# Kernel tuning notes

Measured on AMD Instinct MI355X. Metric: run time of the kernel, lower is better.

Reference implementation:

```python
import jax, jax.numpy as jnp
import numpy as np
import math

B, N, T, F_IN, F_OUT = 8, 512, 12, 32, 64


def setup_inputs() -> dict:
    key = jax.random.key(0)
    k1, k2, k3, k4, k5 = jax.random.split(key, 5)
    x = jax.random.normal(k1, (B, N, T, F_IN), dtype=jnp.float32)
    phaseAct_matrix = jax.random.uniform(k2, (B, T, N, N), dtype=jnp.float32)
    adj = jax.random.uniform(k3, (N, N), dtype=jnp.float32)  # sym-normalized adjacency stand-in
    mask = (jax.random.uniform(k4, (N,)) < 0.5).astype(jnp.float32)  # 1 = observed node, 0 = unknown
    theta = jax.random.normal(k5, (F_IN, F_OUT), dtype=jnp.float32) * 0.05
    return {"x": x, "phaseAct_matrix": phaseAct_matrix, "adj": adj, "mask": mask, "theta": theta}


def _spatial_attention(x):
    # x: (B, N, T, F) -> scores (B, T, N, N)
    f = x.shape[-1]
    xt = x.transpose(0, 2, 1, 3)  # (B, T, N, F)
    score = jnp.einsum('btnf,btmf->btnm', xt, xt) / math.sqrt(f)
    return jax.nn.softmax(score, axis=-1)


def reference(x, phaseAct_matrix, adj, mask, theta):
    f = x.shape[-1]
    t_steps = x.shape[2]
    inv_sqrt_f = 1.0 / math.sqrt(f)
    m = mask[None, :, None, None]  # broadcast over (B, N, T-1, F)

    def body(i, x_cur):
        sa = _spatial_attention(x_cur) * inv_sqrt_f          # (B, T, N, N)
        sat_act = (phaseAct_matrix * sa).transpose(0, 1, 3, 2)  # (B, T, N, N) transposed
        xt = x_cur.transpose(0, 2, 1, 3)                     # (B, T, N, F)
        # predict step t from step t-1: (B, T-1, N, F)
        x_pred = jnp.einsum('btnm,btmf->btnf', sat_act[:, 1:], xt[:, :t_steps - 1])
        x_pred = x_pred.transpose(0, 2, 1, 3)                # (B, N, T-1, F)
        # revise_unknown: keep observed nodes, impute unknown nodes at steps 1..T-1
        x_rev = x_cur[:, :, 1:, :] * m + x_pred * (1.0 - m)
        return jnp.concatenate([x_cur[:, :, 0:1, :], x_rev], axis=2)

    x = jax.lax.fori_loop(1, t_steps, body, x)

    sa = _spatial_attention(x) * inv_sqrt_f                  # (B, T, N, N)
    satAct_adj = phaseAct_matrix * adj[None, None] * sa      # (B, T, N, N)
    xt = x.transpose(0, 2, 1, 3)                             # (B, T, N, F)
    agg = jnp.einsum('btmn,btmf->btnf', satAct_adj, xt)      # transpose(adj) @ x
    out = jax.nn.relu(jnp.einsum('btnf,fo->btno', agg, theta))  # (B, T, N, F_out)
    return out.transpose(0, 2, 1, 3)                         # (B, N, T, F_out)
```

## Files before the change

kernel.cpp:

```cpp
#include <hip/hip_runtime.h>


#define B_ 8
#define N_ 512
#define T_ 12
#define F_ 32
#define O_ 64

typedef unsigned int uint_t;
typedef unsigned short ushort_t;
typedef _Float16 f16_t;
typedef _Float16 f16x4 __attribute__((ext_vector_type(4)));
typedef _Float16 f16x8 __attribute__((ext_vector_type(8)));
typedef float f32x4 __attribute__((ext_vector_type(4)));

__device__ __forceinline__ int xidx(int b, int n, int t, int f) {
    return ((b * N_ + n) * T_ + t) * F_ + f;
}
__device__ __forceinline__ f16x8 load_frag8(const float* p) {
    float4 a = *reinterpret_cast<const float4*>(p);
    float4 b = *reinterpret_cast<const float4*>(p + 4);
    f16x8 r;
    r[0] = (f16_t)a.x; r[1] = (f16_t)a.y; r[2] = (f16_t)a.z; r[3] = (f16_t)a.w;
    r[4] = (f16_t)b.x; r[5] = (f16_t)b.y; r[6] = (f16_t)b.z; r[7] = (f16_t)b.w;
    return r;
}
union U2H4 { uint2 u; f16x4 h; };

__global__ __launch_bounds__(256)
void permute_kernel(const float* __restrict__ src, ushort_t* __restrict__ dst)
{
    __shared__ float Lp[32][516];
    const int tid = threadIdx.x;
    const int cp  = blockIdx.x;
    const int s   = blockIdx.y;
    src += (size_t)s * N_ * N_ + (size_t)cp * 32 * N_;
    uint4* dstu = (uint4*)dst + (size_t)s * 32768 + (size_t)cp * 2048;

    #pragma unroll
    for (int k = 0; k < 64; ++k) {
        int idx = tid + 256 * k;
        Lp[idx >> 9][idx & 511] = src[idx];
    }
    __syncthreads();
    #pragma unroll
    for (int k = 0; k < 8; ++k) {
        int u    = tid + 256 * k;
        int nt   = u >> 6;
        int l    = u & 63;
        int quad = l >> 4;
        int cl   = l & 15;
        int n    = nt * 16 + cl;
        int r0   = quad * 4;
        union { f16_t h[2]; uint_t i; } p0, p1, p2, p3;
        p0.h[0] = (f16_t)Lp[r0][n];      p0.h[1] = (f16_t)Lp[r0 + 1][n];
        p1.h[0] = (f16_t)Lp[r0 + 2][n];  p1.h[1] = (f16_t)Lp[r0 + 3][n];
        p2.h[0] = (f16_t)Lp[16 + r0][n];     p2.h[1] = (f16_t)Lp[16 + r0 + 1][n];
        p3.h[0] = (f16_t)Lp[16 + r0 + 2][n]; p3.h[1] = (f16_t)Lp[16 + r0 + 3][n];
        dstu[u] = make_uint4(p0.i, p1.i, p2.i, p3.i);
    }
}

template <int FINAL>
__global__ __launch_bounds__(256, 4)
void stats_kernel(const float* __restrict__ x0,
                  const float* __restrict__ xcur,
                  float2* __restrict__ MS)
{
    const int tid  = threadIdx.x;
    const int w    = tid >> 6;
    const int l    = tid & 63;
    const int quad = l >> 4;
    const int col  = l & 15;
    const int t    = FINAL ? blockIdx.y : blockIdx.y + 1;
    const int b    = blockIdx.z;
    const int mb   = (blockIdx.x * 4 + w) * 16;
    const float inv_f = 0.17677669529663687f;
    const float* xs = (FINAL && t == 0) ? x0 : xcur;

    f16x8 bm = load_frag8(&xs[xidx(b, mb + col, t, quad * 8)]);

    float M[4] = {-1e30f, -1e30f, -1e30f, -1e30f};
    float S[4] = {0.f, 0.f, 0.f, 0.f};
    #pragma unroll 2
    for (int base = 0; base < 8; ++base) {
        #pragma unroll
        for (int ss = 0; ss < 4; ++ss) {
            const int nt2 = base * 4 + ss;
            f16x8 an = load_frag8(&xs[xidx(b, nt2 * 16 + col, t, quad * 8)]);
            f32x4 s4 = __builtin_amdgcn_mfma_f32_16x16x32_f16(
                           an, bm, (f32x4){0.f, 0.f, 0.f, 0.f}, 0, 0, 0);
            float m4 = fmaxf(fmaxf(s4[0], s4[1]), fmaxf(s4[2], s4[3])) * inv_f;
            float Mn = fmaxf(M[ss], m4);
            S[ss] = S[ss] * __expf(M[ss] - Mn)
                  + (__expf(s4[0] * inv_f - Mn) + __expf(s4[1] * inv_f - Mn))
                  + (__expf(s4[2] * inv_f - Mn) + __expf(s4[3] * inv_f - Mn));
            M[ss] = Mn;
        }
    }
    float M01 = fmaxf(M[0], M[1]);
    float S01 = S[0] * __expf(M[0] - M01) + S[1] * __expf(M[1] - M01);
    float M23 = fmaxf(M[2], M[3]);
    float S23 = S[2] * __expf(M[2] - M23) + S[3] * __expf(M[3] - M23);
    float Mm  = fmaxf(M01, M23);
    float Sm  = S01 * __expf(M01 - Mm) + S23 * __expf(M23 - Mm);
    #pragma unroll
    for (int d = 16; d < 64; d <<= 1) {
        float Mo = __shfl_xor(Mm, d, 64), So = __shfl_xor(Sm, d, 64);
        float Mn = fmaxf(Mm, Mo);
        Sm = Sm * __expf(Mm - Mn) + So * __expf(Mo - Mn);
        Mm = Mn;
    }
    if (l < 16)
        MS[(size_t)(b * T_ + t) * N_ + mb + l] = make_float2(Mm, inv_f / Sm);
}

template <int FINAL>
__global__ __launch_bounds__(256, 3)
void pred_kernel(const float* __restrict__ x0,
                 const float* __restrict__ xcur,
                 float* __restrict__ dst,
                 const ushort_t* __restrict__ phase_h,
                 const ushort_t* __restrict__ adj_h,
                 const float* __restrict__ mask,
                 const float2* __restrict__ MS)
{
    const int tid  = threadIdx.x;
    const int w    = tid >> 6;
    const int l    = tid & 63;
    const int quad = l >> 4;
    const int col  = l & 15;
    const int t    = FINAL ? blockIdx.y : blockIdx.y + 1;
    const int b    = blockIdx.z;
    const int nt   = blockIdx.x * 4 + w;
    const float inv_f = 0.17677669529663687f;

    const float* xs     = (FINAL && t == 0) ? x0 : xcur;
    const float* xp_src = FINAL ? xs : ((t == 1) ? x0 : xcur);
    const int    tp     = FINAL ? t : t - 1;

    f16x8 bf = load_frag8(&xs[xidx(b, nt * 16 + col, t, quad * 8)]);
    const uint4* phu4 = (const uint4*)phase_h + (size_t)(b * T_ + t) * 32768
                        + nt * 64 + l;
    const uint4* adu4 = (const uint4*)adj_h + nt * 64 + l;
    const float2* msp = MS + (size_t)(b * T_ + t) * N_ + quad * 4;

    f32x4 acc0 = (f32x4){0.f, 0.f, 0.f, 0.f};
    f32x4 acc1 = (f32x4){0.f, 0.f, 0.f, 0.f};

    #pragma unroll 2
    for (int cp = 0; cp < 16; ++cp) {
        const int mb0 = cp * 32;
        const int mb1 = mb0 + 16;
        uint4 phq = phu4[cp * 2048];
        uint4 ajq;
        if (FINAL) ajq = adu4[cp * 2048];
        f16x8 af0 = load_frag8(&xs[xidx(b, mb0 + col, t, quad * 8)]);
        f16x8 af1 = load_frag8(&xs[xidx(b, mb1 + col, t, quad * 8)]);
        float4 msA0 = *(const float4*)(msp + mb0);
        float4 msB0 = *(const float4*)(msp + mb0 + 2);
        float4 msA1 = *(const float4*)(msp + mb1);
        float4 msB1 = *(const float4*)(msp + mb1 + 2);
        f16x4 bp00, bp01, bp10, bp11;
        #pragma unroll
        for (int jj = 0; jj < 4; ++jj) {
            bp00[jj] = (f16_t)xp_src[xidx(b, mb0 + quad * 4 + jj, tp, col)];
            bp01[jj] = (f16_t)xp_src[xidx(b, mb0 + quad * 4 + jj, tp, 16 + col)];
            bp10[jj] = (f16_t)xp_src[xidx(b, mb1 + quad * 4 + jj, tp, col)];
            bp11[jj] = (f16_t)xp_src[xidx(b, mb1 + quad * 4 + jj, tp, 16 + col)];
        }

        f32x4 s40 = __builtin_amdgcn_mfma_f32_16x16x32_f16(
                        af0, bf, (f32x4){0.f, 0.f, 0.f, 0.f}, 0, 0, 0);
        f32x4 s41 = __builtin_amdgcn_mfma_f32_16x16x32_f16(
                        af1, bf, (f32x4){0.f, 0.f, 0.f, 0.f}, 0, 0, 0);

        U2H4 p0; p0.u = make_uint2(phq.x, phq.y);
        U2H4 p1; p1.u = make_uint2(phq.z, phq.w);
        U2H4 a0, a1;
        if (FINAL) { a0.u = make_uint2(ajq.x, ajq.y); a1.u = make_uint2(ajq.z, ajq.w); }

        const float Mv0[4] = {msA0.x, msA0.z, msB0.x, msB0.z};
        const float Sv0[4] = {msA0.y, msA0.w, msB0.y, msB0.w};
        const float Mv1[4] = {msA1.x, msA1.z, msB1.x, msB1.z};
        const float Sv1[4] = {msA1.y, msA1.w, msB1.y, msB1.w};

        f16x4 wf0, wf1;
        #pragma unroll
        for (int v = 0; v < 4; ++v) {
            float e0 = __expf(s40[v] * inv_f - Mv0[v]) * Sv0[v] * (float)p0.h[v];
            float e1 = __expf(s41[v] * inv_f - Mv1[v]) * Sv1[v] * (float)p1.h[v];
            if (FINAL) { e0 *= (float)a0.h[v]; e1 *= (float)a1.h[v]; }
            wf0[v] = (f16_t)e0;
            wf1[v] = (f16_t)e1;
        }
        acc0 = __builtin_amdgcn_mfma_f32_16x16x16f16(wf0, bp00, acc0, 0, 0, 0);
        acc1 = __builtin_amdgcn_mfma_f32_16x16x16f16(wf0, bp01, acc1, 0, 0, 0);
        acc0 = __builtin_amdgcn_mfma_f32_16x16x16f16(wf1, bp10, acc0, 0, 0, 0);
        acc1 = __builtin_amdgcn_mfma_f32_16x16x16f16(wf1, bp11, acc1, 0, 0, 0);
    }

    #pragma unroll
    for (int v = 0; v < 4; ++v) {
        const int n = nt * 16 + quad * 4 + v;
        if (FINAL) {
            float* d0 = &dst[((size_t)(b * T_ + t) * N_ + n) * F_ + col];
            d0[0]  = acc0[v];
            d0[16] = acc1[v];
        } else {
            const int i0 = xidx(b, n, t, col);
            const float mk = mask[n];
            dst[i0]      = (mk != 0.f) ? xcur[i0]      : acc0[v];
            dst[i0 + 16] = (mk != 0.f) ? xcur[i0 + 16] : acc1[v];
        }
    }
}

__global__ __launch_bounds__(256)
void proj_kernel(const float* __restrict__ agg, const float* __restrict__ theta,
                 float* __restrict__ out)
{
    __shared__ float th[F_ * O_];
    int tid = threadIdx.x;
    #pragma unroll
    for (int p = 0; p < 8; ++p) th[tid + 256 * p] = theta[tid + 256 * p];
    __syncthreads();
    int g  = blockIdx.x * 256 + tid;
    int o  = g & 63;
    int r  = g >> 6;
    int tt = r % T_;
    int r2 = r / T_;
    int n  = r2 & 511;
    int b  = r2 >> 9;
    const float* a = &agg[((b * T_ + tt) * N_ + n) * F_];
    float s = 0.f;
    #pragma unroll
    for (int f = 0; f < F_; ++f) s += a[f] * th[f * O_ + o];
    out[g] = fmaxf(s, 0.f);
}

extern "C" void kernel_launch(void* const* d_in, const int* in_sizes, int n_in,
                              void* d_out, int out_size, void* d_ws, size_t ws_size,
                              hipStream_t stream)
{
    const float* x     = (const float*)d_in[0];
    const float* phase = (const float*)d_in[1];
    const float* adj   = (const float*)d_in[2];
    const float* mask  = (const float*)d_in[3];
    const float* theta = (const float*)d_in[4];
    float* out = (float*)d_out;

    const size_t XE = (size_t)B_ * N_ * T_ * F_;
    float*    xA      = (float*)d_ws;
    float*    xB      = xA + XE;
    float*    agg     = xB + XE;
    ushort_t* phase_h = (ushort_t*)(agg + XE);
    ushort_t* adj_h   = phase_h + (size_t)96 * N_ * N_;
    float2*   MS      = (float2*)(adj_h + (size_t)N_ * N_);

    permute_kernel<<<dim3(16, 96), 256, 0, stream>>>(phase, phase_h);
    permute_kernel<<<dim3(16, 1), 256, 0, stream>>>(adj, adj_h);

    const float* cur = x;
    float* bufs[2] = { xA, xB };
    for (int i = 0; i < T_ - 1; ++i) {
        float* nxt = bufs[i & 1];
        stats_kernel<0><<<dim3(8, T_ - 1, B_), 256, 0, stream>>>(x, cur, MS);
        pred_kernel<0><<<dim3(8, T_ - 1, B_), 256, 0, stream>>>(
            x, cur, nxt, phase_h, adj_h, mask, MS);
        cur = nxt;
    }
    stats_kernel<1><<<dim3(8, T_, B_), 256, 0, stream>>>(x, cur, MS);
    pred_kernel<1><<<dim3(8, T_, B_), 256, 0, stream>>>(
        x, cur, agg, phase_h, adj_h, mask, MS);
    proj_kernel<<<(B_ * N_ * T_ * O_) / 256, 256, 0, stream>>>(agg, theta, out);
}
```

Baseline: 1.007 ms.

## Fuse softmax stats and prediction kernels with shared-memory row statistics

Merges the softmax statistics kernel into the prediction kernel. Each 512-thread block computes max/sum for all rows of its (b,t) slice into shared memory, then runs the aggregation. This removes a launch per iteration and the global round trip for the stats buffer. In exchange, each block recomputes stats redundantly (4 blocks per slice) and the grid gets smaller and serialized per block.

New measurement: 2.068 ms. +105.3%, slower.

```diff
diff --git a/kernel.cpp b/kernel.cpp
--- a/kernel.cpp
+++ b/kernel.cpp
@@ -62,11 +62,16 @@
 }
 
 template <int FINAL>
-__global__ __launch_bounds__(256, 4)
-void stats_kernel(const float* __restrict__ x0,
+__global__ __launch_bounds__(512, 4)
+void fused_kernel(const float* __restrict__ x0,
                   const float* __restrict__ xcur,
-                  float2* __restrict__ MS)
-{
+                  float* __restrict__ dst,
+                  const ushort_t* __restrict__ phase_h,
+                  const ushort_t* __restrict__ adj_h,
+                  const float* __restrict__ mask)
+{
+    __shared__ float2 MSl[N_];
+
     const int tid  = threadIdx.x;
     const int w    = tid >> 6;
     const int l    = tid & 63;
@@ -74,76 +79,58 @@
     const int col  = l & 15;
     const int t    = FINAL ? blockIdx.y : blockIdx.y + 1;
     const int b    = blockIdx.z;
-    const int mb   = (blockIdx.x * 4 + w) * 16;
-    const float inv_f = 0.17677669529663687f;
-    const float* xs = (FINAL && t == 0) ? x0 : xcur;
-
-    f16x8 bm = load_frag8(&xs[xidx(b, mb + col, t, quad * 8)]);
-
-    float M[4] = {-1e30f, -1e30f, -1e30f, -1e30f};
-    float S[4] = {0.f, 0.f, 0.f, 0.f};
-    #pragma unroll 2
-    for (int base = 0; base < 8; ++base) {
-        #pragma unroll
-        for (int ss = 0; ss < 4; ++ss) {
-            const int nt2 = base * 4 + ss;
-            f16x8 an = load_frag8(&xs[xidx(b, nt2 * 16 + col, t, quad * 8)]);
-            f32x4 s4 = __builtin_amdgcn_mfma_f32_16x16x32_f16(
-                           an, bm, (f32x4){0.f, 0.f, 0.f, 0.f}, 0, 0, 0);
-            float m4 = fmaxf(fmaxf(s4[0], s4[1]), fmaxf(s4[2], s4[3])) * inv_f;
-            float Mn = fmaxf(M[ss], m4);
-            S[ss] = S[ss] * __expf(M[ss] - Mn)
-                  + (__expf(s4[0] * inv_f - Mn) + __expf(s4[1] * inv_f - Mn))
-                  + (__expf(s4[2] * inv_f - Mn) + __expf(s4[3] * inv_f - Mn));
-            M[ss] = Mn;
-        }
-    }
-    float M01 = fmaxf(M[0], M[1]);
-    float S01 = S[0] * __expf(M[0] - M01) + S[1] * __expf(M[1] - M01);
-    float M23 = fmaxf(M[2], M[3]);
-    float S23 = S[2] * __expf(M[2] - M23) + S[3] * __expf(M[3] - M23);
-    float Mm  = fmaxf(M01, M23);
-    float Sm  = S01 * __expf(M01 - Mm) + S23 * __expf(M23 - Mm);
-    #pragma unroll
-    for (int d = 16; d < 64; d <<= 1) {
-        float Mo = __shfl_xor(Mm, d, 64), So = __shfl_xor(Sm, d, 64);
-        float Mn = fmaxf(Mm, Mo);
-        Sm = Sm * __expf(Mm - Mn) + So * __expf(Mo - Mn);
-        Mm = Mn;
-    }
-    if (l < 16)
-        MS[(size_t)(b * T_ + t) * N_ + mb + l] = make_float2(Mm, inv_f / Sm);
-}
-
-template <int FINAL>
-__global__ __launch_bounds__(256, 3)
-void pred_kernel(const float* __restrict__ x0,
-                 const float* __restrict__ xcur,
-                 float* __restrict__ dst,
-                 const ushort_t* __restrict__ phase_h,
-                 const ushort_t* __restrict__ adj_h,
-                 const float* __restrict__ mask,
-                 const float2* __restrict__ MS)
-{
-    const int tid  = threadIdx.x;
-    const int w    = tid >> 6;
-    const int l    = tid & 63;
-    const int quad = l >> 4;
-    const int col  = l & 15;
-    const int t    = FINAL ? blockIdx.y : blockIdx.y + 1;
-    const int b    = blockIdx.z;
-    const int nt   = blockIdx.x * 4 + w;
     const float inv_f = 0.17677669529663687f;
 
     const float* xs     = (FINAL && t == 0) ? x0 : xcur;
     const float* xp_src = FINAL ? xs : ((t == 1) ? x0 : xcur);
     const int    tp     = FINAL ? t : t - 1;
 
+    for (int mi = 0; mi < 4; ++mi) {
+        const int mb = (w * 4 + mi) * 16;
+        f16x8 bm = load_frag8(&xs[xidx(b, mb + col, t, quad * 8)]);
+
+        float M[4] = {-1e30f, -1e30f, -1e30f, -1e30f};
+        float S[4] = {0.f, 0.f, 0.f, 0.f};
+        #pragma unroll 2
+        for (int base = 0; base < 8; ++base) {
+            #pragma unroll
+            for (int ss = 0; ss < 4; ++ss) {
+                const int nt2 = base * 4 + ss;
+                f16x8 an = load_frag8(&xs[xidx(b, nt2 * 16 + col, t, quad * 8)]);
+                f32x4 s4 = __builtin_amdgcn_mfma_f32_16x16x32_f16(
+                               an, bm, (f32x4){0.f, 0.f, 0.f, 0.f}, 0, 0, 0);
+                float m4 = fmaxf(fmaxf(s4[0], s4[1]), fmaxf(s4[2], s4[3])) * inv_f;
+                float Mn = fmaxf(M[ss], m4);
+                S[ss] = S[ss] * __expf(M[ss] - Mn)
+                      + (__expf(s4[0] * inv_f - Mn) + __expf(s4[1] * inv_f - Mn))
+                      + (__expf(s4[2] * inv_f - Mn) + __expf(s4[3] * inv_f - Mn));
+                M[ss] = Mn;
+            }
+        }
+        float M01 = fmaxf(M[0], M[1]);
+        float S01 = S[0] * __expf(M[0] - M01) + S[1] * __expf(M[1] - M01);
+        float M23 = fmaxf(M[2], M[3]);
+        float S23 = S[2] * __expf(M[2] - M23) + S[3] * __expf(M[3] - M23);
+        float Mm  = fmaxf(M01, M23);
+        float Sm  = S01 * __expf(M01 - Mm) + S23 * __expf(M23 - Mm);
+        #pragma unroll
+        for (int d = 16; d < 64; d <<= 1) {
+            float Mo = __shfl_xor(Mm, d, 64), So = __shfl_xor(Sm, d, 64);
+            float Mn = fmaxf(Mm, Mo);
+            Sm = Sm * __expf(Mm - Mn) + So * __expf(Mo - Mn);
+            Mm = Mn;
+        }
+        if (l < 16)
+            MSl[mb + l] = make_float2(Mm, inv_f / Sm);
+    }
+    __syncthreads();
+
+    const int nt = blockIdx.x * 8 + w;
     f16x8 bf = load_frag8(&xs[xidx(b, nt * 16 + col, t, quad * 8)]);
     const uint4* phu4 = (const uint4*)phase_h + (size_t)(b * T_ + t) * 32768
                         + nt * 64 + l;
     const uint4* adu4 = (const uint4*)adj_h + nt * 64 + l;
-    const float2* msp = MS + (size_t)(b * T_ + t) * N_ + quad * 4;
+    const float* msp = (const float*)MSl + quad * 8;
 
     f32x4 acc0 = (f32x4){0.f, 0.f, 0.f, 0.f};
     f32x4 acc1 = (f32x4){0.f, 0.f, 0.f, 0.f};
@@ -157,10 +144,10 @@
         if (FINAL) ajq = adu4[cp * 2048];
         f16x8 af0 = load_frag8(&xs[xidx(b, mb0 + col, t, quad * 8)]);
         f16x8 af1 = load_frag8(&xs[xidx(b, mb1 + col, t, quad * 8)]);
-        float4 msA0 = *(const float4*)(msp + mb0);
-        float4 msB0 = *(const float4*)(msp + mb0 + 2);
-        float4 msA1 = *(const float4*)(msp + mb1);
-        float4 msB1 = *(const float4*)(msp + mb1 + 2);
+        float4 msA0 = *(const float4*)(msp + mb0 * 2);
+        float4 msB0 = *(const float4*)(msp + mb0 * 2 + 4);
+        float4 msA1 = *(const float4*)(msp + mb1 * 2);
+        float4 msB1 = *(const float4*)(msp + mb1 * 2 + 4);
         f16x4 bp00, bp01, bp10, bp11;
         #pragma unroll
         for (int jj = 0; jj < 4; ++jj) {
@@ -256,7 +243,6 @@
     float*    agg     = xB + XE;
     ushort_t* phase_h = (ushort_t*)(agg + XE);
     ushort_t* adj_h   = phase_h + (size_t)96 * N_ * N_;
-    float2*   MS      = (float2*)(adj_h + (size_t)N_ * N_);
 
     permute_kernel<<<dim3(16, 96), 256, 0, stream>>>(phase, phase_h);
     permute_kernel<<<dim3(16, 1), 256, 0, stream>>>(adj, adj_h);
@@ -265,13 +251,11 @@
     float* bufs[2] = { xA, xB };
     for (int i = 0; i < T_ - 1; ++i) {
         float* nxt = bufs[i & 1];
-        stats_kernel<0><<<dim3(8, T_ - 1, B_), 256, 0, stream>>>(x, cur, MS);
-        pred_kernel<0><<<dim3(8, T_ - 1, B_), 256, 0, stream>>>(
-            x, cur, nxt, phase_h, adj_h, mask, MS);
+        fused_kernel<0><<<dim3(4, T_ - 1, B_), 512, 0, stream>>>(
+            x, cur, nxt, phase_h, adj_h, mask);
         cur = nxt;
     }
-    stats_kernel<1><<<dim3(8, T_, B_), 256, 0, stream>>>(x, cur, MS);
-    pred_kernel<1><<<dim3(8, T_, B_), 256, 0, stream>>>(
-        x, cur, agg, phase_h, adj_h, mask, MS);
+    fused_kernel<1><<<dim3(4, T_, B_), 512, 0, stream>>>(
+        x, cur, agg, phase_h, adj_h, mask);
     proj_kernel<<<(B_ * N_ * T_ * O_) / 256, 256, 0, stream>>>(agg, theta, out);
 }
```

## Software-pipeline global loads in stats and aggregation kernels with register prefetch

Applied to the files above, without the earlier changes.

The stats kernel now keeps a four-deep ring of x fragments in registers and issues the load for tile nt+4 before the MFMA for tile nt. The aggregation kernel is fully unrolled over 32 column tiles with double-buffered staging of x, softmax stats and the previous-step features. Phase and adjacency values are prefetched eight tiles ahead. The aim is to hide global-load latency behind MFMA and exp work, at the cost of higher register pressure and possibly lower occupancy.

Result: faster. 936.9 us (-7.0%).

```diff
diff --git a/kernel.cpp b/kernel.cpp
--- a/kernel.cpp
+++ b/kernel.cpp
@@ -17,13 +17,15 @@
 __device__ __forceinline__ int xidx(int b, int n, int t, int f) {
     return ((b * N_ + n) * T_ + t) * F_ + f;
 }
-__device__ __forceinline__ f16x8 load_frag8(const float* p) {
-    float4 a = *reinterpret_cast<const float4*>(p);
-    float4 b = *reinterpret_cast<const float4*>(p + 4);
+__device__ __forceinline__ f16x8 cvt_frag8(float4 a, float4 b) {
     f16x8 r;
     r[0] = (f16_t)a.x; r[1] = (f16_t)a.y; r[2] = (f16_t)a.z; r[3] = (f16_t)a.w;
     r[4] = (f16_t)b.x; r[5] = (f16_t)b.y; r[6] = (f16_t)b.z; r[7] = (f16_t)b.w;
     return r;
+}
+__device__ __forceinline__ f16x8 load_frag8(const float* p) {
+    return cvt_frag8(*reinterpret_cast<const float4*>(p),
+                     *reinterpret_cast<const float4*>(p + 4));
 }
 union U2H4 { uint2 u; f16x4 h; };
 
@@ -80,23 +82,34 @@
 
     f16x8 bm = load_frag8(&xs[xidx(b, mb + col, t, quad * 8)]);
 
+    float4 xr[4][2];
+    #pragma unroll
+    for (int p = 0; p < 4; ++p) {
+        const float* ap = &xs[xidx(b, p * 16 + col, t, quad * 8)];
+        xr[p][0] = *reinterpret_cast<const float4*>(ap);
+        xr[p][1] = *reinterpret_cast<const float4*>(ap + 4);
+    }
+
     float M[4] = {-1e30f, -1e30f, -1e30f, -1e30f};
     float S[4] = {0.f, 0.f, 0.f, 0.f};
-    #pragma unroll 2
-    for (int base = 0; base < 8; ++base) {
-        #pragma unroll
-        for (int ss = 0; ss < 4; ++ss) {
-            const int nt2 = base * 4 + ss;
-            f16x8 an = load_frag8(&xs[xidx(b, nt2 * 16 + col, t, quad * 8)]);
-            f32x4 s4 = __builtin_amdgcn_mfma_f32_16x16x32_f16(
-                           an, bm, (f32x4){0.f, 0.f, 0.f, 0.f}, 0, 0, 0);
-            float m4 = fmaxf(fmaxf(s4[0], s4[1]), fmaxf(s4[2], s4[3])) * inv_f;
-            float Mn = fmaxf(M[ss], m4);
-            S[ss] = S[ss] * __expf(M[ss] - Mn)
-                  + (__expf(s4[0] * inv_f - Mn) + __expf(s4[1] * inv_f - Mn))
-                  + (__expf(s4[2] * inv_f - Mn) + __expf(s4[3] * inv_f - Mn));
-            M[ss] = Mn;
-        }
+    #pragma unroll
+    for (int nt2 = 0; nt2 < 32; ++nt2) {
+        const int rb = nt2 & 3;
+        f16x8 an = cvt_frag8(xr[rb][0], xr[rb][1]);
+        if (nt2 + 4 < 32) {
+            const float* ap = &xs[xidx(b, (nt2 + 4) * 16 + col, t, quad * 8)];
+            xr[rb][0] = *reinterpret_cast<const float4*>(ap);
+            xr[rb][1] = *reinterpret_cast<const float4*>(ap + 4);
+        }
+        f32x4 s4 = __builtin_amdgcn_mfma_f32_16x16x32_f16(
+                       an, bm, (f32x4){0.f, 0.f, 0.f, 0.f}, 0, 0, 0);
+        const int ss = rb;
+        float m4 = fmaxf(fmaxf(s4[0], s4[1]), fmaxf(s4[2], s4[3])) * inv_f;
+        float Mn = fmaxf(M[ss], m4);
+        S[ss] = S[ss] * __expf(M[ss] - Mn)
+              + (__expf(s4[0] * inv_f - Mn) + __expf(s4[1] * inv_f - Mn))
+              + (__expf(s4[2] * inv_f - Mn) + __expf(s4[3] * inv_f - Mn));
+        M[ss] = Mn;
     }
     float M01 = fmaxf(M[0], M[1]);
     float S01 = S[0] * __expf(M[0] - M01) + S[1] * __expf(M[1] - M01);
@@ -140,65 +153,82 @@
     const int    tp     = FINAL ? t : t - 1;
 
     f16x8 bf = load_frag8(&xs[xidx(b, nt * 16 + col, t, quad * 8)]);
-    const uint4* phu4 = (const uint4*)phase_h + (size_t)(b * T_ + t) * 32768
-                        + nt * 64 + l;
-    const uint4* adu4 = (const uint4*)adj_h + nt * 64 + l;
-    const float2* msp = MS + (size_t)(b * T_ + t) * N_ + quad * 4;
+    const uint2* phu2 = (const uint2*)((const uint4*)phase_h
+                        + (size_t)(b * T_ + t) * 32768 + nt * 64 + l);
+    const uint2* adu2 = (const uint2*)((const uint4*)adj_h + nt * 64 + l);
+    const float* msp  = (const float*)(MS + (size_t)(b * T_ + t) * N_) + quad * 8;
 
     f32x4 acc0 = (f32x4){0.f, 0.f, 0.f, 0.f};
     f32x4 acc1 = (f32x4){0.f, 0.f, 0.f, 0.f};
 
-    #pragma unroll 2
-    for (int cp = 0; cp < 16; ++cp) {
-        const int mb0 = cp * 32;
-        const int mb1 = mb0 + 16;
-        uint4 phq = phu4[cp * 2048];
-        uint4 ajq;
-        if (FINAL) ajq = adu4[cp * 2048];
-        f16x8 af0 = load_frag8(&xs[xidx(b, mb0 + col, t, quad * 8)]);
-        f16x8 af1 = load_frag8(&xs[xidx(b, mb1 + col, t, quad * 8)]);
-        float4 msA0 = *(const float4*)(msp + mb0);
-        float4 msB0 = *(const float4*)(msp + mb0 + 2);
-        float4 msA1 = *(const float4*)(msp + mb1);
-        float4 msB1 = *(const float4*)(msp + mb1 + 2);
-        f16x4 bp00, bp01, bp10, bp11;
+    uint2  ph[8], aj[8];
+    float4 xr[2][2];
+    float4 msr[2][2];
+    float  bpr[2][8];
+
+#define PH_LD(c)  phu2[(size_t)((c) >> 1) * 4096 + ((c) & 1)]
+#define AD_LD(c)  adu2[(size_t)((c) >> 1) * 4096 + ((c) & 1)]
+#define STAGE(s, c)                                                          \
+    {                                                                        \
+        const float* ap_ = &xs[xidx(b, (c) * 16 + col, t, quad * 8)];        \
+        xr[s][0] = *reinterpret_cast<const float4*>(ap_);                    \
+        xr[s][1] = *reinterpret_cast<const float4*>(ap_ + 4);                \
+        msr[s][0] = *reinterpret_cast<const float4*>(msp + (c) * 32);        \
+        msr[s][1] = *reinterpret_cast<const float4*>(msp + (c) * 32 + 4);    \
+        _Pragma("unroll")                                                    \
+        for (int jj = 0; jj < 4; ++jj) {                                     \
+            const int r_ = (c) * 16 + quad * 4 + jj;                         \
+            bpr[s][jj]     = xp_src[xidx(b, r_, tp, col)];                   \
+            bpr[s][4 + jj] = xp_src[xidx(b, r_, tp, 16 + col)];              \
+        }                                                                    \
+    }
+
+    #pragma unroll
+    for (int p = 0; p < 8; ++p) {
+        ph[p] = PH_LD(p);
+        if (FINAL) aj[p] = AD_LD(p);
+    }
+    STAGE(0, 0);
+
+    #pragma unroll
+    for (int c = 0; c < 32; ++c) {
+        const int cur = c & 1, nxt = cur ^ 1, rb = c & 7;
+        if (c < 31) STAGE(nxt, c + 1);
+        uint2 phq = ph[rb];
+        if (c + 8 < 32) ph[rb] = PH_LD(c + 8);
+        uint2 ajq;
+        if (FINAL) {
+            ajq = aj[rb];
+            if (c + 8 < 32) aj[rb] = AD_LD(c + 8);
+        }
+
+        f16x8 af = cvt_frag8(xr[cur][0], xr[cur][1]);
+        f32x4 s4 = __builtin_amdgcn_mfma_f32_16x16x32_f16(
+                       af, bf, (f32x4){0.f, 0.f, 0.f, 0.f}, 0, 0, 0);
+
+        const float Mv[4] = {msr[cur][0].x, msr[cur][0].z, msr[cur][1].x, msr[cur][1].z};
+        const float Sv[4] = {msr[cur][0].y, msr[cur][0].w, msr[cur][1].y, msr[cur][1].w};
+        U2H4 p0; p0.u = phq;
+        U2H4 a0; if (FINAL) a0.u = ajq;
+        f16x4 wf;
+        #pragma unroll
+        for (int v = 0; v < 4; ++v) {
+            float e = __expf(s4[v] * inv_f - Mv[v]) * Sv[v] * (float)p0.h[v];
+            if (FINAL) e *= (float)a0.h[v];
+            wf[v] = (f16_t)e;
+        }
+        f16x4 bp0, bp1;
         #pragma unroll
         for (int jj = 0; jj < 4; ++jj) {
-            bp00[jj] = (f16_t)xp_src[xidx(b, mb0 + quad * 4 + jj, tp, col)];
-            bp01[jj] = (f16_t)xp_src[xidx(b, mb0 + quad * 4 + jj, tp, 16 + col)];
-            bp10[jj] = (f16_t)xp_src[xidx(b, mb1 + quad * 4 + jj, tp, col)];
-            bp11[jj] = (f16_t)xp_src[xidx(b, mb1 + quad * 4 + jj, tp, 16 + col)];
-        }
-
-        f32x4 s40 = __builtin_amdgcn_mfma_f32_16x16x32_f16(
-                        af0, bf, (f32x4){0.f, 0.f, 0.f, 0.f}, 0, 0, 0);
-        f32x4 s41 = __builtin_amdgcn_mfma_f32_16x16x32_f16(
-                        af1, bf, (f32x4){0.f, 0.f, 0.f, 0.f}, 0, 0, 0);
-
-        U2H4 p0; p0.u = make_uint2(phq.x, phq.y);
-        U2H4 p1; p1.u = make_uint2(phq.z, phq.w);
-        U2H4 a0, a1;
-        if (FINAL) { a0.u = make_uint2(ajq.x, ajq.y); a1.u = make_uint2(ajq.z, ajq.w); }
-
-        const float Mv0[4] = {msA0.x, msA0.z, msB0.x, msB0.z};
-        const float Sv0[4] = {msA0.y, msA0.w, msB0.y, msB0.w};
-        const float Mv1[4] = {msA1.x, msA1.z, msB1.x, msB1.z};
-        const float Sv1[4] = {msA1.y, msA1.w, msB1.y, msB1.w};
-
-        f16x4 wf0, wf1;
-        #pragma unroll
-        for (int v = 0; v < 4; ++v) {
-            float e0 = __expf(s40[v] * inv_f - Mv0[v]) * Sv0[v] * (float)p0.h[v];
-            float e1 = __expf(s41[v] * inv_f - Mv1[v]) * Sv1[v] * (float)p1.h[v];
-            if (FINAL) { e0 *= (float)a0.h[v]; e1 *= (float)a1.h[v]; }
-            wf0[v] = (f16_t)e0;
-            wf1[v] = (f16_t)e1;
-        }
-        acc0 = __builtin_amdgcn_mfma_f32_16x16x16f16(wf0, bp00, acc0, 0, 0, 0);
-        acc1 = __builtin_amdgcn_mfma_f32_16x16x16f16(wf0, bp01, acc1, 0, 0, 0);
-        acc0 = __builtin_amdgcn_mfma_f32_16x16x16f16(wf1, bp10, acc0, 0, 0, 0);
-        acc1 = __builtin_amdgcn_mfma_f32_16x16x16f16(wf1, bp11, acc1, 0, 0, 0);
-    }
+            bp0[jj] = (f16_t)bpr[cur][jj];
+            bp1[jj] = (f16_t)bpr[cur][4 + jj];
+        }
+        acc0 = __builtin_amdgcn_mfma_f32_16x16x16f16(wf, bp0, acc0, 0, 0, 0);
+        acc1 = __builtin_amdgcn_mfma_f32_16x16x16f16(wf, bp1, acc1, 0, 0, 0);
+    }
+#undef PH_LD
+#undef AD_LD
+#undef STAGE
 
     #pragma unroll
     for (int v = 0; v < 4; ++v) {
```
